# Kernel tuning notes

Hardware: AMD Instinct MI355X
Metric: run time of the kernel (lower is better)

The kernel has to match this reference:

```python
import jax, jax.numpy as jnp
import numpy as np

LEAK = 0.01  # torch LeakyReLU default negative_slope
HALF_LOG_2PI = 0.5 * float(np.log(2.0 * np.pi))


def setup_inputs() -> dict:
    key = jax.random.key(0)
    ks = jax.random.split(key, 5)
    N, D = 8192, 512
    H = 2 * D
    x = jax.random.normal(ks[0], (N, D), dtype=jnp.float32)
    # small init so exp(logvar/2) stays well-behaved (mimics trained-net scale)
    W1 = jax.random.normal(ks[1], (H, H), dtype=jnp.float32) * 0.02
    b1 = jnp.zeros((H,), dtype=jnp.float32)
    W2 = jax.random.normal(ks[2], (H, H), dtype=jnp.float32) * 0.02
    b2 = jnp.zeros((H,), dtype=jnp.float32)
    eps = jax.random.normal(ks[3], (N, D), dtype=jnp.float32)
    return {"x": x, "W1": W1, "b1": b1, "W2": W2, "b2": b2, "eps": eps, "n": 4}


def reference(x, W1, b1, W2, b2, eps, n):
    N, D = x.shape
    # pairwise squared distances via the expansion identity (avoids [N,N,D] diff)
    sq = jnp.sum(x * x, axis=1)                       # [N]
    d = sq[:, None] + sq[None, :] - 2.0 * (x @ x.T)   # [N, N]
    # argsort(d)[:, :n] == indices of the n smallest distances per row
    _, subsets = jax.lax.top_k(-d, n)                 # [N, n]
    z = x[subsets]                                    # [N, n, D] gather
    mu_pool = jnp.mean(z, axis=1)                     # [N, D]
    mx_pool = jnp.max(z, axis=1)                      # [N, D]
    h = jnp.concatenate((mu_pool, mx_pool), axis=1)   # [N, 2D]
    # decoder: Linear -> LeakyReLU -> Linear (torch Linear: h @ W.T + b)
    h = h @ W1.T + b1
    h = jnp.where(h >= 0, h, LEAK * h)
    h = h @ W2.T + b2
    mu = h[:, :D]
    sigma = jnp.exp(h[:, D:] * 0.5)
    x_out = x + mu + sigma * eps                      # rsample
    entropy = jnp.mean(0.5 + HALF_LOG_2PI + jnp.log(sigma))
    rows = jnp.repeat(jnp.arange(N), n)
    sub_idx = (rows, subsets.reshape(-1))
    return (x_out, entropy, sub_idx)
```

## Files before the change

### kernel.cpp

```cpp
#include <hip/hip_runtime.h>
#include <math.h>

#define N_ROWS 8192
#define DIM 512
#define HID 1024

typedef _Float16 f16x8 __attribute__((ext_vector_type(8)));
typedef _Float16 f16x4 __attribute__((ext_vector_type(4)));
typedef float f32x4 __attribute__((ext_vector_type(4)));

__device__ __forceinline__ bool dj_less(float d1, int j1, float d2, int j2) {
  return (d1 < d2) || (d1 == d2 && j1 < j2);
}
__device__ __forceinline__ unsigned umin32(unsigned a, unsigned b) { return a < b ? a : b; }
__device__ __forceinline__ unsigned umax32(unsigned a, unsigned b) { return a > b ? a : b; }

__device__ __forceinline__ void gload_lds16(const void* g, void* s) {
  __builtin_amdgcn_global_load_lds((const __attribute__((address_space(1))) void*)g,
                                   (__attribute__((address_space(3))) void*)s, 16, 0, 0);
}

#define S_SWZ(r) ((((r) & 3) ^ (((r) >> 2) & 3)))

#define INS4(K, xin)                                   \
  {                                                    \
    unsigned xx = (xin), t;                            \
    t = umin32(K[0], xx); xx = umax32(K[0], xx); K[0] = t; \
    t = umin32(K[1], xx); xx = umax32(K[1], xx); K[1] = t; \
    t = umin32(K[2], xx); xx = umax32(K[2], xx); K[2] = t; \
    K[3] = umin32(K[3], xx);                           \
  }

__global__ __launch_bounds__(256) void convert_kernel(const float* __restrict__ x,
                                                      const float* __restrict__ W1,
                                                      const float* __restrict__ W2,
                                                      _Float16* __restrict__ xh,
                                                      _Float16* __restrict__ W1f,
                                                      _Float16* __restrict__ W2f,
                                                      float* __restrict__ sq) {
  int bid = blockIdx.x;
  int tid = threadIdx.x;
  if (bid < 4096) {
    int g = bid * 256 + tid;
    float4 v = reinterpret_cast<const float4*>(x)[g];
    f16x4 hv = {(_Float16)v.x, (_Float16)v.y, (_Float16)v.z, (_Float16)v.w};
    reinterpret_cast<f16x4*>(xh)[g] = hv;
    float s = v.x * v.x + v.y * v.y + v.z * v.z + v.w * v.w;
    for (int off = 32; off > 0; off >>= 1) s += __shfl_down(s, off);
    __shared__ float red[4];
    if ((tid & 63) == 0) red[tid >> 6] = s;
    __syncthreads();
    if (tid == 0) sq[bid * 2] = red[0] + red[1];
    if (tid == 128) sq[bid * 2 + 1] = red[2] + red[3];
  } else {
    const float* src = (bid < 5120) ? W1 : W2;
    _Float16* dst = (bid < 5120) ? W1f : W2f;
    int g = ((bid < 5120) ? (bid - 4096) : (bid - 5120)) * 256 + tid;
    float4 v = reinterpret_cast<const float4*>(src)[g];
    f16x4 h = {(_Float16)v.x, (_Float16)v.y, (_Float16)v.z, (_Float16)v.w};
    reinterpret_cast<f16x4*>(dst)[g] = h;
  }
}

__global__ __launch_bounds__(256, 4) void dist_sym_mfma(const _Float16* __restrict__ xh,
                                                        const float* __restrict__ sq,
                                                        unsigned int* __restrict__ cand) {
  __shared__ __align__(16) char smem[34048];
  unsigned* DkA = (unsigned*)(smem);
  unsigned* DkB = (unsigned*)(smem + 17024);
  unsigned* Tk = (unsigned*)(smem);
  const int tid = threadIdx.x;
  const int lane = tid & 63;
  const int w = tid >> 6;
  const int wm = w >> 1, wn = w & 1;
  const int lo = lane & 15, hi = lane >> 4;

  int It, Jt;
  {
    int bid = blockIdx.x;
    int rem = (bid & 7) * 260 + (bid >> 3);
    int SI = 0, SJ = 0;
#pragma unroll 1
    for (int s = 0; s < 36; ++s) {
      int cnt = (SI == SJ) ? 36 : 64;
      if (rem < cnt) break;
      rem -= cnt;
      ++SJ;
      if (SJ == 8) { ++SI; SJ = SI; }
    }
    int ii, jj;
    if (SI == SJ) {
      ii = 0;
      int c = 8;
      while (rem >= c) { rem -= c; ++ii; c = 8 - ii; }
      jj = ii + rem;
    } else {
      ii = rem >> 3;
      jj = rem & 7;
    }
    It = SI * 8 + ii;
    Jt = SJ * 8 + jj;
  }

  int a_off[4], b_off[4];
#pragma unroll
  for (int m = 0; m < 4; ++m) {
    int r = wm * 64 + m * 16 + lo;
    a_off[m] = r * 64 + (((lane >> 4) ^ S_SWZ(r)) * 16);
  }
#pragma unroll
  for (int n = 0; n < 4; ++n) {
    int r = wn * 64 + n * 16 + lo;
    b_off[n] = r * 64 + (((lane >> 4) ^ S_SWZ(r)) * 16);
  }

  int goff[2], wb[2];
#pragma unroll
  for (int h = 0; h < 2; ++h) {
    int i = h * 256 + tid;
    int r = i >> 2, cs = i & 3;
    int c = cs ^ S_SWZ(r);
    goff[h] = r * 512 + c * 8;
    wb[h] = h * 4096 + w * 1024;
  }

  const int slot = wn * 16 + lo;

  const _Float16* arow = xh + (size_t)(It * 128) * DIM;
  const _Float16* brow = xh + (size_t)(Jt * 128) * DIM;

  f32x4 acc[4][4];
#pragma unroll
  for (int m = 0; m < 4; ++m)
#pragma unroll
    for (int n = 0; n < 4; ++n) acc[m][n] = (f32x4)0.0f;

  auto stage = [&](int b, int kt) {
#pragma unroll
    for (int h = 0; h < 2; ++h) {
      int go = goff[h] + kt * 32;
      gload_lds16(arow + go, smem + b * 16384 + wb[h]);
      gload_lds16(brow + go, smem + b * 16384 + 8192 + wb[h]);
    }
  };
  auto compute = [&](int b) {
    f16x8 bf[4];
#pragma unroll
    for (int n = 0; n < 4; ++n) bf[n] = *(const f16x8*)(smem + b * 16384 + 8192 + b_off[n]);
#pragma unroll
    for (int m = 0; m < 4; ++m) {
      f16x8 af = *(const f16x8*)(smem + b * 16384 + a_off[m]);
#pragma unroll
      for (int n = 0; n < 4; ++n)
        acc[m][n] = __builtin_amdgcn_mfma_f32_16x16x32_f16(af, bf[n], acc[m][n], 0, 0, 0);
    }
  };

  stage(0, 0);
  __syncthreads();
#pragma unroll 1
  for (int k = 0; k < 8; ++k) {
    stage(1, 2 * k + 1);
    compute(0);
    __syncthreads();
    if (k < 7) stage(0, 2 * k + 2);
    compute(1);
    __syncthreads();
  }

  float sqjb[4];
#pragma unroll
  for (int n = 0; n < 4; ++n) sqjb[n] = sq[Jt * 128 + wn * 64 + n * 16 + lo] + 1024.0f;

  unsigned Kj[4][4];
#pragma unroll
  for (int n = 0; n < 4; ++n)
#pragma unroll
    for (int q = 0; q < 4; ++q) Kj[n][q] = 0xFFFFFFFFu;

#pragma unroll
  for (int m = 0; m < 4; ++m) {
    float sqr_m[4];
#pragma unroll
    for (int j = 0; j < 4; ++j)
      sqr_m[j] = sq[It * 128 + wm * 64 + m * 16 + hi * 4 + j] + 1024.0f;
#pragma unroll
    for (int j = 0; j < 4; ++j) {
      int rl = wm * 64 + m * 16 + hi * 4 + j;
      unsigned u[4];
#pragma unroll
      for (int n = 0; n < 4; ++n) {
        float vi = fmaf(-2.0f, acc[m][n][j], sqjb[n]);
        u[n] = (__float_as_uint(vi) & 0xFFFFE000u) |
               (unsigned)(Jt * 128 + wn * 64 + n * 16 + lo);
        float vj = fmaf(-2.0f, acc[m][n][j], sqr_m[j]);
        unsigned kt = (__float_as_uint(vj) & 0xFFFFE000u) | (unsigned)(It * 128 + rl);
        INS4(Kj[n], kt);
      }
      unsigned lo01 = umin32(u[0], u[1]), hi01 = umax32(u[0], u[1]);
      unsigned lo23 = umin32(u[2], u[3]), hi23 = umax32(u[2], u[3]);
      DkA[slot * 133 + rl] = umin32(lo01, lo23);
      DkB[slot * 133 + rl] = umin32(umax32(lo01, lo23), umin32(hi01, hi23));
    }
  }
  __syncthreads();

  if (tid < 128) {
    unsigned K4[4] = {0xFFFFFFFFu, 0xFFFFFFFFu, 0xFFFFFFFFu, 0xFFFFFFFFu};
#pragma unroll
    for (int s = 0; s < 32; ++s) {
      INS4(K4, DkA[s * 133 + tid]);
      INS4(K4, DkB[s * 133 + tid]);
    }
    uint4 o;
    o.x = K4[0]; o.y = K4[1]; o.z = K4[2]; o.w = K4[3];
    *reinterpret_cast<uint4*>(&cand[((size_t)Jt * N_ROWS + It * 128 + tid) * 4]) = o;
  }

  if (It != Jt) {
    __syncthreads();
#pragma unroll
    for (int n = 0; n < 4; ++n) {
      int coll = wn * 64 + n * 16 + lo;
#pragma unroll
      for (int q = 0; q < 4; ++q)
        Tk[((wm * 4 + hi) * 4 + q) * 133 + coll] = Kj[n][q];
    }
    __syncthreads();
    if (tid < 128) {
      unsigned K4[4] = {0xFFFFFFFFu, 0xFFFFFFFFu, 0xFFFFFFFFu, 0xFFFFFFFFu};
#pragma unroll
      for (int s = 0; s < 32; ++s) INS4(K4, Tk[s * 133 + tid]);
      uint4 o;
      o.x = K4[0]; o.y = K4[1]; o.z = K4[2]; o.w = K4[3];
      *reinterpret_cast<uint4*>(&cand[((size_t)It * N_ROWS + Jt * 128 + tid) * 4]) = o;
    }
  }
}

__global__ __launch_bounds__(256) void rescore_pool_kernel(const float* __restrict__ x,
                                                           const float* __restrict__ sq,
                                                           const unsigned int* __restrict__ cand,
                                                           float* __restrict__ orows,
                                                           float* __restrict__ osubs,
                                                           _Float16* __restrict__ h0) {
  const int lane = threadIdx.x & 63;
  const int wid = threadIdx.x >> 6;
  const int row = blockIdx.x * 4 + wid;
  uint4 q = *reinterpret_cast<const uint4*>(&cand[((size_t)lane * N_ROWS + row) * 4]);
  unsigned cur = q.x, c1 = q.y, c2 = q.z, c3 = q.w;
  unsigned myj = 0;
#pragma unroll 1
  for (int r = 0; r < 16; ++r) {
    unsigned mn = cur;
#pragma unroll
    for (int off = 32; off > 0; off >>= 1)
      mn = umin32(mn, (unsigned)__shfl_xor((int)mn, off));
    if (cur == mn) { cur = c1; c1 = c2; c2 = c3; c3 = 0xFFFFFFFFu; }
    if (lane == r) myj = mn & 0x1FFFu;
  }

  const float4* xi = reinterpret_cast<const float4*>(x + (size_t)row * DIM);
  float4 xa = xi[lane];
  float4 xb = xi[lane + 64];
  float sqi = sq[row];

  float dme = 0.0f;
  int jme = 0;
#pragma unroll 1
  for (int c = 0; c < 16; ++c) {
    int j = __shfl((int)myj, c);
    const float4* xj = reinterpret_cast<const float4*>(x + (size_t)j * DIM);
    float4 ya = xj[lane];
    float4 yb = xj[lane + 64];
    float dot = xa.x * ya.x + xa.y * ya.y + xa.z * ya.z + xa.w * ya.w +
                xb.x * yb.x + xb.y * yb.y + xb.z * yb.z + xb.w * yb.w;
#pragma unroll
    for (int off = 32; off > 0; off >>= 1) dot += __shfl_xor(dot, off);
    float d = sqi + sq[j] - 2.0f * dot;
    if (lane == c) { dme = d; jme = j; }
  }

  int rank2 = 0;
#pragma unroll
  for (int k = 0; k < 16; ++k) {
    float dk = __shfl(dme, k);
    int jk = __shfl(jme, k);
    rank2 += dj_less(dk, jk, dme, jme) ? 1 : 0;
  }
  __shared__ int s4[4][4];
  if (lane < 16 && rank2 < 4) {
    s4[wid][rank2] = jme;
    orows[row * 4 + rank2] = (float)row;
    osubs[row * 4 + rank2] = (float)jme;
  }
  __syncthreads();

  int j0 = s4[wid][0], j1 = s4[wid][1], j2 = s4[wid][2], j3 = s4[wid][3];
  int c = lane * 8;
  float4 z0a = *reinterpret_cast<const float4*>(&x[(size_t)j0 * DIM + c]);
  float4 z0b = *reinterpret_cast<const float4*>(&x[(size_t)j0 * DIM + c + 4]);
  float4 z1a = *reinterpret_cast<const float4*>(&x[(size_t)j1 * DIM + c]);
  float4 z1b = *reinterpret_cast<const float4*>(&x[(size_t)j1 * DIM + c + 4]);
  float4 z2a = *reinterpret_cast<const float4*>(&x[(size_t)j2 * DIM + c]);
  float4 z2b = *reinterpret_cast<const float4*>(&x[(size_t)j2 * DIM + c + 4]);
  float4 z3a = *reinterpret_cast<const float4*>(&x[(size_t)j3 * DIM + c]);
  float4 z3b = *reinterpret_cast<const float4*>(&x[(size_t)j3 * DIM + c + 4]);
  f16x8 mu, mx;
  mu[0] = (_Float16)((z0a.x + z1a.x + z2a.x + z3a.x) * 0.25f);
  mu[1] = (_Float16)((z0a.y + z1a.y + z2a.y + z3a.y) * 0.25f);
  mu[2] = (_Float16)((z0a.z + z1a.z + z2a.z + z3a.z) * 0.25f);
  mu[3] = (_Float16)((z0a.w + z1a.w + z2a.w + z3a.w) * 0.25f);
  mu[4] = (_Float16)((z0b.x + z1b.x + z2b.x + z3b.x) * 0.25f);
  mu[5] = (_Float16)((z0b.y + z1b.y + z2b.y + z3b.y) * 0.25f);
  mu[6] = (_Float16)((z0b.z + z1b.z + z2b.z + z3b.z) * 0.25f);
  mu[7] = (_Float16)((z0b.w + z1b.w + z2b.w + z3b.w) * 0.25f);
  mx[0] = (_Float16)fmaxf(fmaxf(z0a.x, z1a.x), fmaxf(z2a.x, z3a.x));
  mx[1] = (_Float16)fmaxf(fmaxf(z0a.y, z1a.y), fmaxf(z2a.y, z3a.y));
  mx[2] = (_Float16)fmaxf(fmaxf(z0a.z, z1a.z), fmaxf(z2a.z, z3a.z));
  mx[3] = (_Float16)fmaxf(fmaxf(z0a.w, z1a.w), fmaxf(z2a.w, z3a.w));
  mx[4] = (_Float16)fmaxf(fmaxf(z0b.x, z1b.x), fmaxf(z2b.x, z3b.x));
  mx[5] = (_Float16)fmaxf(fmaxf(z0b.y, z1b.y), fmaxf(z2b.y, z3b.y));
  mx[6] = (_Float16)fmaxf(fmaxf(z0b.z, z1b.z), fmaxf(z2b.z, z3b.z));
  mx[7] = (_Float16)fmaxf(fmaxf(z0b.w, z1b.w), fmaxf(z2b.w, z3b.w));
  *reinterpret_cast<f16x8*>(&h0[(size_t)row * HID + c]) = mu;
  *reinterpret_cast<f16x8*>(&h0[(size_t)row * HID + DIM + c]) = mx;
}

__global__ __launch_bounds__(256, 2) void gemm_mfma_kernel(const _Float16* __restrict__ A,
                                                           const _Float16* __restrict__ W,
                                                           const float* __restrict__ bias,
                                                           _Float16* __restrict__ out16,
                                                           int act) {
  __shared__ __align__(16) char smem[32768];
  const int tid = threadIdx.x;
  const int lane = tid & 63;
  const int w = tid >> 6;
  const int wm = w >> 1, wn = w & 1;
  const int row0 = blockIdx.x * 128;
  const int col0 = blockIdx.y * 128;

  int a_off[4], b_off[4];
#pragma unroll
  for (int m = 0; m < 4; ++m) {
    int r = wm * 64 + m * 16 + (lane & 15);
    a_off[m] = r * 64 + (((lane >> 4) ^ S_SWZ(r)) * 16);
  }
#pragma unroll
  for (int n = 0; n < 4; ++n) {
    int r = wn * 64 + n * 16 + (lane & 15);
    b_off[n] = r * 64 + (((lane >> 4) ^ S_SWZ(r)) * 16);
  }

  int goff[2], wb[2];
#pragma unroll
  for (int h = 0; h < 2; ++h) {
    int i = h * 256 + tid;
    int r = i >> 2, cs = i & 3;
    int c = cs ^ S_SWZ(r);
    goff[h] = r * HID + c * 8;
    wb[h] = h * 4096 + w * 1024;
  }

  const _Float16* arow = A + (size_t)row0 * HID;
  const _Float16* brow = W + (size_t)col0 * HID;

  f32x4 acc[4][4];
#pragma unroll
  for (int m = 0; m < 4; ++m)
#pragma unroll
    for (int n = 0; n < 4; ++n) acc[m][n] = (f32x4)0.0f;

  auto stage = [&](int b, int kt) {
#pragma unroll
    for (int h = 0; h < 2; ++h) {
      int go = goff[h] + kt * 32;
      gload_lds16(arow + go, smem + b * 16384 + wb[h]);
      gload_lds16(brow + go, smem + b * 16384 + 8192 + wb[h]);
    }
  };
  auto compute = [&](int b) {
    f16x8 bf[4];
#pragma unroll
    for (int n = 0; n < 4; ++n) bf[n] = *(const f16x8*)(smem + b * 16384 + 8192 + b_off[n]);
#pragma unroll
    for (int m = 0; m < 4; ++m) {
      f16x8 af = *(const f16x8*)(smem + b * 16384 + a_off[m]);
#pragma unroll
      for (int n = 0; n < 4; ++n)
        acc[m][n] = __builtin_amdgcn_mfma_f32_16x16x32_f16(af, bf[n], acc[m][n], 0, 0, 0);
    }
  };

  stage(0, 0);
  __syncthreads();
#pragma unroll 1
  for (int k = 0; k < 16; ++k) {
    stage(1, 2 * k + 1);
    compute(0);
    __syncthreads();
    if (k < 15) stage(0, 2 * k + 2);
    compute(1);
    __syncthreads();
  }

  float bv[4];
#pragma unroll
  for (int n = 0; n < 4; ++n) bv[n] = bias[col0 + wn * 64 + n * 16 + (lane & 15)];

#pragma unroll
  for (int m = 0; m < 4; ++m)
#pragma unroll
    for (int n = 0; n < 4; ++n) {
      int cl = col0 + wn * 64 + n * 16 + (lane & 15);
#pragma unroll
      for (int j = 0; j < 4; ++j) {
        int rl = row0 + wm * 64 + m * 16 + ((lane >> 4) << 2) + j;
        float v = acc[m][n][j] + bv[n];
        if (act && v < 0.0f) v *= 0.01f;
        out16[(size_t)rl * HID + cl] = (_Float16)v;
      }
    }
}

__global__ __launch_bounds__(256) void outgen_kernel(const float* __restrict__ x,
                                                     const _Float16* __restrict__ h2,
                                                     const float* __restrict__ eps,
                                                     float* __restrict__ xout,
                                                     float* __restrict__ partials) {
  int tid = threadIdx.x;
  int gid = blockIdx.x * 256 + tid;
  size_t base = (size_t)gid * 4;
  int i = (int)(base >> 9);
  int c = (int)(base & 511);
  float4 xv = *reinterpret_cast<const float4*>(&x[base]);
  float4 ev = *reinterpret_cast<const float4*>(&eps[base]);
  f16x4 muh = *reinterpret_cast<const f16x4*>(&h2[(size_t)i * HID + c]);
  f16x4 hsh = *reinterpret_cast<const f16x4*>(&h2[(size_t)i * HID + DIM + c]);
  float hs0 = (float)hsh[0], hs1 = (float)hsh[1], hs2 = (float)hsh[2], hs3 = (float)hsh[3];
  float4 xo;
  xo.x = xv.x + (float)muh[0] + expf(0.5f * hs0) * ev.x;
  xo.y = xv.y + (float)muh[1] + expf(0.5f * hs1) * ev.y;
  xo.z = xv.z + (float)muh[2] + expf(0.5f * hs2) * ev.z;
  xo.w = xv.w + (float)muh[3] + expf(0.5f * hs3) * ev.w;
  *reinterpret_cast<float4*>(&xout[base]) = xo;
  float lsum = hs0 + hs1 + hs2 + hs3;
  for (int off = 32; off > 0; off >>= 1) lsum += __shfl_down(lsum, off);
  __shared__ float red[4];
  if ((tid & 63) == 0) red[tid >> 6] = lsum;
  __syncthreads();
  if (tid == 0) partials[blockIdx.x] = red[0] + red[1] + red[2] + red[3];
}

__global__ __launch_bounds__(256) void entfin_kernel(const float* __restrict__ partials,
                                                     float* __restrict__ ent) {
  int t = threadIdx.x;
  float s = 0.0f;
  for (int q = 0; q < 16; ++q) s += partials[t + 256 * q];
  for (int off = 32; off > 0; off >>= 1) s += __shfl_down(s, off);
  __shared__ float red[4];
  if ((t & 63) == 0) red[t >> 6] = s;
  __syncthreads();
  if (t == 0)
    ent[0] = 0.5f + 0.9189385332046727f +
             0.5f * (red[0] + red[1] + red[2] + red[3]) / (8192.0f * 512.0f);
}

extern "C" void kernel_launch(void* const* d_in, const int* in_sizes, int n_in,
                              void* d_out, int out_size, void* d_ws, size_t ws_size,
                              hipStream_t stream) {
  const float* x = (const float*)d_in[0];
  const float* W1 = (const float*)d_in[1];
  const float* b1 = (const float*)d_in[2];
  const float* W2 = (const float*)d_in[3];
  const float* b2 = (const float*)d_in[4];
  const float* eps = (const float*)d_in[5];

  float* out = (float*)d_out;
  float* ws = (float*)d_ws;

  float* sq = ws;
  float* partials = ws + 40960;
  unsigned int* cand = (unsigned int*)(ws + 65536);
  _Float16* h2f = (_Float16*)(ws + 65536);
  _Float16* xh = (_Float16*)(ws + 8454144);
  _Float16* h0f = (_Float16*)(ws + 8454144);
  _Float16* h1f = (_Float16*)(ws + 12648448);
  _Float16* W1f = (_Float16*)(ws + 16842752);
  _Float16* W2f = (_Float16*)(ws + 17367040);

  float* xout = out;
  float* ent = out + (size_t)N_ROWS * DIM;
  float* orows = ent + 1;
  float* osubs = orows + (size_t)N_ROWS * 4;

  convert_kernel<<<6144, 256, 0, stream>>>(x, W1, W2, xh, W1f, W2f, sq);
  dist_sym_mfma<<<2080, 256, 0, stream>>>(xh, sq, cand);
  rescore_pool_kernel<<<N_ROWS / 4, 256, 0, stream>>>(x, sq, cand, orows, osubs, h0f);
  gemm_mfma_kernel<<<dim3(64, 8), 256, 0, stream>>>(h0f, W1f, b1, h1f, 1);
  gemm_mfma_kernel<<<dim3(64, 8), 256, 0, stream>>>(h1f, W2f, b2, h2f, 0);
  outgen_kernel<<<4096, 256, 0, stream>>>(x, h2f, eps, xout, partials);
  entfin_kernel<<<1, 256, 0, stream>>>(partials, ent);
}
```

Before: 161.9 us.

## Double GEMM K-tile to 64 and parallelize candidate distance refinement across lanes

The MFMA GEMM now stages 64-wide K tiles (64KB LDS double buffer, 8-way XOR swizzle), which halves the number of barriers and loop iterations. The cost is that LDS per block rises to 64KB, which may cut occupancy below the two blocks requested in launch bounds. The candidate refinement in the gather kernel now computes all 16 distances at once, with four lanes per candidate each doing a serial FMA dot product over a quarter row. This replaces 16 sequential full-wave reductions but makes each lane's global reads strided and uncoalesced.

Result: slower. 200.6 us (+23.9%).

```diff
diff --git a/kernel.cpp b/kernel.cpp
--- a/kernel.cpp
+++ b/kernel.cpp
@@ -260,36 +260,34 @@
     if (lane == r) myj = mn & 0x1FFFu;
   }
 
-  const float4* xi = reinterpret_cast<const float4*>(x + (size_t)row * DIM);
-  float4 xa = xi[lane];
-  float4 xb = xi[lane + 64];
-  float sqi = sq[row];
-
-  float dme = 0.0f;
-  int jme = 0;
-#pragma unroll 1
-  for (int c = 0; c < 16; ++c) {
-    int j = __shfl((int)myj, c);
-    const float4* xj = reinterpret_cast<const float4*>(x + (size_t)j * DIM);
-    float4 ya = xj[lane];
-    float4 yb = xj[lane + 64];
-    float dot = xa.x * ya.x + xa.y * ya.y + xa.z * ya.z + xa.w * ya.w +
-                xb.x * yb.x + xb.y * yb.y + xb.z * yb.z + xb.w * yb.w;
-#pragma unroll
-    for (int off = 32; off > 0; off >>= 1) dot += __shfl_xor(dot, off);
-    float d = sqi + sq[j] - 2.0f * dot;
-    if (lane == c) { dme = d; jme = j; }
-  }
+  const int ci = lane >> 2, part = lane & 3;
+  int j = __shfl((int)myj, ci);
+  const float4* xi = reinterpret_cast<const float4*>(x + (size_t)row * DIM) + part * 32;
+  const float4* xj = reinterpret_cast<const float4*>(x + (size_t)j * DIM) + part * 32;
+  float dot = 0.0f;
+#pragma unroll
+  for (int t = 0; t < 32; ++t) {
+    float4 a = xi[t];
+    float4 b = xj[t];
+    dot = fmaf(a.x, b.x, dot);
+    dot = fmaf(a.y, b.y, dot);
+    dot = fmaf(a.z, b.z, dot);
+    dot = fmaf(a.w, b.w, dot);
+  }
+  dot += __shfl_xor(dot, 1);
+  dot += __shfl_xor(dot, 2);
+  float dme = sq[row] + sq[j] - 2.0f * dot;
+  int jme = j;
 
   int rank2 = 0;
 #pragma unroll
   for (int k = 0; k < 16; ++k) {
-    float dk = __shfl(dme, k);
-    int jk = __shfl(jme, k);
+    float dk = __shfl(dme, k * 4);
+    int jk = __shfl(jme, k * 4);
     rank2 += dj_less(dk, jk, dme, jme) ? 1 : 0;
   }
   __shared__ int s4[4][4];
-  if (lane < 16 && rank2 < 4) {
+  if (part == 0 && rank2 < 4) {
     s4[wid][rank2] = jme;
     orows[row * 4 + rank2] = (float)row;
     osubs[row * 4 + rank2] = (float)jme;
@@ -332,32 +330,37 @@
                                                            const float* __restrict__ bias,
                                                            _Float16* __restrict__ out16,
                                                            int act) {
-  __shared__ __align__(16) char smem[32768];
+  __shared__ __align__(16) char smem[65536];
   const int tid = threadIdx.x;
   const int lane = tid & 63;
   const int w = tid >> 6;
   const int wm = w >> 1, wn = w & 1;
+  const int lo = lane & 15, hi = lane >> 4;
   const int row0 = blockIdx.x * 128;
   const int col0 = blockIdx.y * 128;
 
-  int a_off[4], b_off[4];
+  int a_off[4][2], b_off[4][2];
 #pragma unroll
   for (int m = 0; m < 4; ++m) {
-    int r = wm * 64 + m * 16 + (lane & 15);
-    a_off[m] = r * 64 + (((lane >> 4) ^ S_SWZ(r)) * 16);
+    int r = wm * 64 + m * 16 + lo;
+#pragma unroll
+    for (int ks = 0; ks < 2; ++ks)
+      a_off[m][ks] = r * 128 + (((ks * 4 + hi) ^ (r & 7)) * 16);
   }
 #pragma unroll
   for (int n = 0; n < 4; ++n) {
-    int r = wn * 64 + n * 16 + (lane & 15);
-    b_off[n] = r * 64 + (((lane >> 4) ^ S_SWZ(r)) * 16);
-  }
-
-  int goff[2], wb[2];
-#pragma unroll
-  for (int h = 0; h < 2; ++h) {
+    int r = wn * 64 + n * 16 + lo;
+#pragma unroll
+    for (int ks = 0; ks < 2; ++ks)
+      b_off[n][ks] = r * 128 + (((ks * 4 + hi) ^ (r & 7)) * 16);
+  }
+
+  int goff[4], wb[4];
+#pragma unroll
+  for (int h = 0; h < 4; ++h) {
     int i = h * 256 + tid;
-    int r = i >> 2, cs = i & 3;
-    int c = cs ^ S_SWZ(r);
+    int r = i >> 3, cs = i & 7;
+    int c = cs ^ (r & 7);
     goff[h] = r * HID + c * 8;
     wb[h] = h * 4096 + w * 1024;
   }
@@ -373,49 +376,53 @@
 
   auto stage = [&](int b, int kt) {
 #pragma unroll
-    for (int h = 0; h < 2; ++h) {
-      int go = goff[h] + kt * 32;
-      gload_lds16(arow + go, smem + b * 16384 + wb[h]);
-      gload_lds16(brow + go, smem + b * 16384 + 8192 + wb[h]);
+    for (int h = 0; h < 4; ++h) {
+      int go = goff[h] + kt * 64;
+      gload_lds16(arow + go, smem + b * 32768 + wb[h]);
+      gload_lds16(brow + go, smem + b * 32768 + 16384 + wb[h]);
     }
   };
   auto compute = [&](int b) {
-    f16x8 bf[4];
-#pragma unroll
-    for (int n = 0; n < 4; ++n) bf[n] = *(const f16x8*)(smem + b * 16384 + 8192 + b_off[n]);
-#pragma unroll
-    for (int m = 0; m < 4; ++m) {
-      f16x8 af = *(const f16x8*)(smem + b * 16384 + a_off[m]);
+#pragma unroll
+    for (int ks = 0; ks < 2; ++ks) {
+      f16x8 bf[4];
 #pragma unroll
       for (int n = 0; n < 4; ++n)
-        acc[m][n] = __builtin_amdgcn_mfma_f32_16x16x32_f16(af, bf[n], acc[m][n], 0, 0, 0);
+        bf[n] = *(const f16x8*)(smem + b * 32768 + 16384 + b_off[n][ks]);
+#pragma unroll
+      for (int m = 0; m < 4; ++m) {
+        f16x8 af = *(const f16x8*)(smem + b * 32768 + a_off[m][ks]);
+#pragma unroll
+        for (int n = 0; n < 4; ++n)
+          acc[m][n] = __builtin_amdgcn_mfma_f32_16x16x32_f16(af, bf[n], acc[m][n], 0, 0, 0);
+      }
     }
   };
 
   stage(0, 0);
   __syncthreads();
 #pragma unroll 1
-  for (int k = 0; k < 16; ++k) {
+  for (int k = 0; k < 8; ++k) {
     stage(1, 2 * k + 1);
     compute(0);
     __syncthreads();
-    if (k < 15) stage(0, 2 * k + 2);
+    if (k < 7) stage(0, 2 * k + 2);
     compute(1);
     __syncthreads();
   }
 
   float bv[4];
 #pragma unroll
-  for (int n = 0; n < 4; ++n) bv[n] = bias[col0 + wn * 64 + n * 16 + (lane & 15)];
+  for (int n = 0; n < 4; ++n) bv[n] = bias[col0 + wn * 64 + n * 16 + lo];
 
 #pragma unroll
   for (int m = 0; m < 4; ++m)
 #pragma unroll
     for (int n = 0; n < 4; ++n) {
-      int cl = col0 + wn * 64 + n * 16 + (lane & 15);
+      int cl = col0 + wn * 64 + n * 16 + lo;
 #pragma unroll
       for (int j = 0; j < 4; ++j) {
-        int rl = row0 + wm * 64 + m * 16 + ((lane >> 4) << 2) + j;
+        int rl = row0 + wm * 64 + m * 16 + hi * 4 + j;
         float v = acc[m][n][j] + bv[n];
         if (act && v < 0.0f) v *= 0.01f;
         out16[(size_t)rl * HID + cl] = (_Float16)v;
```
